# Kernel tuning notes

Measured on AMD Instinct MI355X. Metric: run time of the kernel, lower is better.

The kernel has to match this reference:

```python
import jax, jax.numpy as jnp
import numpy as np

V = 32000   # shared src/trg vocab size
E = 128     # EMB_DIM
H = 256     # HID_DIM
B = 32      # batch
S = 64      # src len
T = 64      # trg len


def setup_inputs() -> dict:
    key = jax.random.key(0)
    ks = jax.random.split(key, 16)
    s = 0.05
    n = lambda k, shape: jax.random.normal(k, shape, dtype=jnp.float32) * s
    return {
        "src": jax.random.randint(ks[0], (B, S), 0, V),
        "trg": jax.random.randint(ks[1], (B, T), 0, V),
        "enc_emb": n(ks[2], (V, E)),
        "enc_Wih": n(ks[3], (4 * H, E)),
        "enc_Whh": n(ks[4], (4 * H, H)),
        "enc_b": n(ks[5], (4 * H,)),   # b_ih + b_hh fused
        "dec_emb": n(ks[6], (V, E)),
        "dec_Wih": n(ks[7], (4 * H, E)),
        "dec_Whh": n(ks[8], (4 * H, H)),
        "dec_b": n(ks[9], (4 * H,)),
        "fc_W": n(ks[10], (V, H)),
        "fc_b": n(ks[11], (V,)),
    }


def _lstm_scan(x_seq, h0, c0, Wih, Whh, b):
    # x_seq: [T, B, E]; PyTorch gate order: i, f, g, o
    def step(carry, x):
        h, c = carry
        gates = x @ Wih.T + h @ Whh.T + b          # [B, 4H]
        i, f, g, o = jnp.split(gates, 4, axis=-1)
        c = jax.nn.sigmoid(f) * c + jax.nn.sigmoid(i) * jnp.tanh(g)
        h = jax.nn.sigmoid(o) * jnp.tanh(c)
        return (h, c), h
    (h, c), hs = jax.lax.scan(step, (h0, c0), x_seq)
    return h, c, hs


def reference(src, trg, enc_emb, enc_Wih, enc_Whh, enc_b,
              dec_emb, dec_Wih, dec_Whh, dec_b, fc_W, fc_b):
    dtype = enc_emb.dtype
    h0 = jnp.zeros((B, H), dtype)
    c0 = jnp.zeros((B, H), dtype)

    # Encoder: embed src, run LSTM, keep final (hidden, cell)
    src_e = enc_emb[src].transpose(1, 0, 2)        # [S, B, E]
    h, c, _ = _lstm_scan(src_e, h0, c0, enc_Wih, enc_Whh, enc_b)

    # Decoder with teacher_forcing_ratio=1.0: input at step t is trg[:, t-1]
    dec_in = dec_emb[trg[:, :-1]].transpose(1, 0, 2)   # [T-1, B, E]
    _, _, hs = _lstm_scan(dec_in, h, c, dec_Wih, dec_Whh, dec_b)  # [T-1, B, H]

    logits = hs @ fc_W.T + fc_b                    # [T-1, B, V]
    # outputs[:, 0, :] stays zero as in the torch code
    outputs = jnp.concatenate(
        [jnp.zeros((1, B, fc_W.shape[0]), dtype), logits], axis=0)
    return outputs.transpose(1, 0, 2)              # [B, T, V]
```

## Files before the change

kernel.cpp:

```cpp
#include <hip/hip_runtime.h>


typedef _Float16 f16x2 __attribute__((ext_vector_type(2)));
typedef short short8 __attribute__((ext_vector_type(8)));
typedef float f32x4 __attribute__((ext_vector_type(4)));
typedef unsigned long long u64;

#define DEV __device__ __forceinline__

static constexpr int Vv = 32000, Ee = 128, Hh = 256, Bb = 32, Ss = 64, Tt = 64;
static constexpr int G4 = 4 * Hh;
static constexpr int MR = (Tt - 1) * Bb;
static constexpr size_t OUT_BT = (size_t)Tt * Vv;

static constexpr size_t OFF_ENCPRE = 0;
static constexpr size_t OFF_DECPRE = OFF_ENCPRE + (size_t)Ss * Bb * G4 * 4;
static constexpr size_t OFF_WQE    = OFF_DECPRE + (size_t)(Tt - 1) * Bb * G4 * 4;
static constexpr size_t OFF_WQD    = OFF_WQE + (size_t)G4 * Hh * 2;
static constexpr size_t OFF_WPE    = OFF_WQD + (size_t)G4 * Hh * 2;
static constexpr size_t OFF_WPD    = OFF_WPE + (size_t)G4 * Ee * 4;
static constexpr size_t OFF_HW     = OFF_WPD + (size_t)G4 * Ee * 4;

DEV float sigm(float x) { return 1.0f / (1.0f + expf(-x)); }

DEV unsigned short f2bf(float x) {
  unsigned u = __float_as_uint(x);
  u = u + 0x7fffu + ((u >> 16) & 1u);
  return (unsigned short)(u >> 16);
}

DEV float dot2(unsigned wu, unsigned hu, float acc) {
  union { unsigned u; f16x2 v; } a, b;
  a.u = wu; b.u = hu;
#if __has_builtin(__builtin_amdgcn_fdot2)
  return __builtin_amdgcn_fdot2(a.v, b.v, acc, false);
#else
  return acc + (float)a.v.x * (float)b.v.x + (float)a.v.y * (float)b.v.y;
#endif
}

__global__ __launch_bounds__(256) void k_pack_whh(const float* __restrict__ src,
                                                  _Float16* __restrict__ dst) {
  int tid = blockIdx.x * 256 + threadIdx.x;
  if (tid >= G4 * Hh) return;
  int r = tid >> 8, k = tid & 255;
  dst[((size_t)(k >> 3) * G4 + r) * 8 + (k & 7)] = (_Float16)src[tid];
}

__global__ __launch_bounds__(256) void k_pack_wih(const float* __restrict__ src,
                                                  float* __restrict__ dst) {
  int tid = blockIdx.x * 256 + threadIdx.x;
  if (tid >= G4 * Ee) return;
  int g = tid >> 7, e = tid & 127;
  dst[((size_t)(e >> 2) * G4 + g) * 4 + (e & 3)] = src[tid];
}

__global__ __launch_bounds__(256) void k_init(u64* __restrict__ w) {
  w[blockIdx.x * 256 + threadIdx.x] = 0ull;
}

__global__ __launch_bounds__(1024) void k_pre(
    const int* __restrict__ src, const int* __restrict__ trg,
    const float* __restrict__ enc_emb, const float* __restrict__ dec_emb,
    const float* __restrict__ WpE, const float* __restrict__ WpD,
    const float* __restrict__ enc_b, const float* __restrict__ dec_b,
    float* __restrict__ enc_pre, float* __restrict__ dec_pre) {
  int blk = blockIdx.x;
  int step = blk >> 2;
  int b0 = (blk & 3) * 8;
  bool enc = step < Ss;
  int ts = enc ? step : step - Ss;
  const int*   tok  = enc ? src : trg;
  const float* emb  = enc ? enc_emb : dec_emb;
  const float* Wp   = enc ? WpE : WpD;
  const float* bias = enc ? enc_b : dec_b;
  float* pre = enc ? (enc_pre + ((size_t)step * Bb + b0) * G4)
                   : (dec_pre + ((size_t)(step - Ss) * Bb + b0) * G4);

  __shared__ __align__(16) float xs[8][128];
  int tid = threadIdx.x;
  {
    int bl = tid >> 7, e = tid & 127;
    int token = tok[(b0 + bl) * 64 + ts];
    xs[bl][e] = emb[(size_t)token * Ee + e];
  }
  __syncthreads();

  int g = tid;
  float acc[8];
  float bv = bias[g];
#pragma unroll
  for (int bb = 0; bb < 8; ++bb) acc[bb] = bv;

  const f32x4* w4 = (const f32x4*)Wp;
  const f32x4(*x4)[32] = (const f32x4(*)[32])xs;
#pragma unroll 4
  for (int e4 = 0; e4 < 32; ++e4) {
    f32x4 w = w4[(size_t)e4 * G4 + g];
#pragma unroll
    for (int bb = 0; bb < 8; ++bb) {
      f32x4 xv = x4[bb][e4];
      acc[bb] += w.x * xv.x + w.y * xv.y + w.z * xv.z + w.w * xv.w;
    }
  }
#pragma unroll
  for (int bb = 0; bb < 8; ++bb) pre[(size_t)bb * G4 + g] = acc[bb];
}

__global__ __launch_bounds__(256, 1) void k_lstm2(
    const float* __restrict__ enc_pre, const float* __restrict__ dec_pre,
    const _Float16* __restrict__ WqE, const _Float16* __restrict__ WqD,
    u64* __restrict__ hword, float* __restrict__ hs) {
  const int bid = blockIdx.x;
  const int j = bid >> 5, b = bid & 31;
  const int t = threadIdx.x;
  const int wv = t >> 6, l = t & 63;
  const int c_loc = l & 31, khalf = l >> 5;
  const int r_loc = wv * 32 + c_loc;
  const int row = wv * 256 + j * 32 + c_loc;

  __shared__ uint4 wlds[2][32][128];
  __shared__ unsigned hbits[128];
  __shared__ float gbuf[4][32];
  __shared__ float hstash[32];

  {
    const uint4* gE = (const uint4*)WqE + row;
    const uint4* gD = (const uint4*)WqD + row;
#pragma unroll 4
    for (int kk = 0; kk < 32; ++kk) wlds[0][kk][r_loc] = gE[(size_t)kk * G4];
#pragma unroll 4
    for (int kk = 0; kk < 32; ++kk) wlds[1][kk][r_loc] = gD[(size_t)kk * G4];
  }
  float c = 0.0f;
  __syncthreads();

  for (int step = 0; step < 127; ++step) {
    const bool enc = step < Ss;
    const float* pre = (enc ? enc_pre + (size_t)step * (Bb * G4)
                            : dec_pre + (size_t)(step - Ss) * (Bb * G4)) +
                       (size_t)b * G4;
    float pv = pre[row];

    if (t < 128) {
      if (step == 0) {
        hbits[t] = 0u;
      } else {
        u64* wp = hword + ((size_t)(step & 1) * 32 + b) * 128 + t;
        u64 v;
        do {
          v = __hip_atomic_load(wp, __ATOMIC_RELAXED, __HIP_MEMORY_SCOPE_AGENT);
        } while ((unsigned)(v >> 32) != (unsigned)step);
        hbits[t] = (unsigned)v;
      }
    }
    __syncthreads();

    const uint4* wl = &wlds[enc ? 0 : 1][khalf * 16][0];
    const uint4* hv4 = (const uint4*)hbits;
    float a0 = 0.f, a1 = 0.f, a2 = 0.f, a3 = 0.f;
#pragma unroll
    for (int k8 = 0; k8 < 16; ++k8) {
      uint4 w8 = wl[k8 * 128 + r_loc];
      uint4 h8 = hv4[khalf * 16 + k8];
      a0 = dot2(w8.x, h8.x, a0);
      a1 = dot2(w8.y, h8.y, a1);
      a2 = dot2(w8.z, h8.z, a2);
      a3 = dot2(w8.w, h8.w, a3);
    }
    float acc = (a0 + a1) + (a2 + a3);
    acc += __shfl_xor(acc, 32, 64);
    if (l < 32) gbuf[wv][c_loc] = acc + pv;
    __syncthreads();

    if (t < 32) {
      float gi = gbuf[0][t], gf = gbuf[1][t], gg = gbuf[2][t], go = gbuf[3][t];
      c = sigm(gf) * c + sigm(gi) * tanhf(gg);
      float hn = sigm(go) * tanhf(c);
      hstash[t] = hn;
      if (!enc) hs[((size_t)(step - Ss) * Bb + b) * Hh + j * 32 + t] = hn;
      if ((t & 1) == 0) {
        union { _Float16 f; unsigned short u; } u0, u1;
        u0.f = (_Float16)hn;
        u1.f = (_Float16)hstash[t + 1];
        u64 wd = ((u64)(unsigned)(step + 1) << 32) |
                 ((unsigned)u1.u << 16) | (unsigned)u0.u;
        __hip_atomic_store(
            hword + ((size_t)((step + 1) & 1) * 32 + b) * 128 + j * 16 + (t >> 1),
            wd, __ATOMIC_RELAXED, __HIP_MEMORY_SCOPE_AGENT);
      }
    }
  }
}

__global__ __launch_bounds__(256) void k_zero0(float* __restrict__ out) {
  int v = blockIdx.x * 256 + threadIdx.x;
  out[(size_t)blockIdx.y * OUT_BT + v] = 0.0f;
}

__global__ __launch_bounds__(256) void k_fc(const float* __restrict__ hs,
                                            const float* __restrict__ fcW,
                                            const float* __restrict__ fcb,
                                            float* __restrict__ out) {
  constexpr int LDH = 136;
  __shared__ __align__(16) unsigned short As[64 * LDH];
  __shared__ __align__(16) unsigned short Bs[64 * LDH];
  int n0 = blockIdx.x * 64, m0 = blockIdx.y * 64;
  int tid = threadIdx.x;
  int lane = tid & 63, wave = tid >> 6;
  int l15 = lane & 15, q = lane >> 4;
  int msub = (wave & 1) * 32, nsub = (wave >> 1) * 32;
  f32x4 acc[2][2] = {};

  for (int kb = 0; kb < 2; ++kb) {
#pragma unroll
    for (int r = 0; r < 4; ++r) {
      int vecid = tid + 256 * r;
      int i = vecid >> 4;
      int kk = (vecid & 15) * 8;
      int gk = kb * 128 + kk;
      short8 va, vb;
      int gm = m0 + i;
      if (gm < MR) {
        const float* p = hs + (size_t)gm * Hh + gk;
#pragma unroll
        for (int e = 0; e < 8; ++e) va[e] = (short)f2bf(p[e]);
      } else {
#pragma unroll
        for (int e = 0; e < 8; ++e) va[e] = 0;
      }
      const float* pb = fcW + (size_t)(n0 + i) * Hh + gk;
#pragma unroll
      for (int e = 0; e < 8; ++e) vb[e] = (short)f2bf(pb[e]);
      *(short8*)&As[i * LDH + kk] = va;
      *(short8*)&Bs[i * LDH + kk] = vb;
    }
    __syncthreads();
#pragma unroll
    for (int ks = 0; ks < 4; ++ks) {
      int koff = ks * 32 + q * 8;
      short8 a0 = *(const short8*)&As[(msub + l15) * LDH + koff];
      short8 a1 = *(const short8*)&As[(msub + 16 + l15) * LDH + koff];
      short8 b0 = *(const short8*)&Bs[(nsub + l15) * LDH + koff];
      short8 b1 = *(const short8*)&Bs[(nsub + 16 + l15) * LDH + koff];
      acc[0][0] = __builtin_amdgcn_mfma_f32_16x16x32_bf16(a0, b0, acc[0][0], 0, 0, 0);
      acc[0][1] = __builtin_amdgcn_mfma_f32_16x16x32_bf16(a0, b1, acc[0][1], 0, 0, 0);
      acc[1][0] = __builtin_amdgcn_mfma_f32_16x16x32_bf16(a1, b0, acc[1][0], 0, 0, 0);
      acc[1][1] = __builtin_amdgcn_mfma_f32_16x16x32_bf16(a1, b1, acc[1][1], 0, 0, 0);
    }
    __syncthreads();
  }
#pragma unroll
  for (int ni = 0; ni < 2; ++ni) {
    int gn = n0 + nsub + ni * 16 + l15;
    float bv = fcb[gn];
#pragma unroll
    for (int mi = 0; mi < 2; ++mi) {
#pragma unroll
      for (int r = 0; r < 4; ++r) {
        int gm = m0 + msub + mi * 16 + q * 4 + r;
        if (gm < MR) {
          int tt = gm >> 5, bb = gm & 31;
          out[(size_t)bb * OUT_BT + (size_t)(tt + 1) * Vv + gn] = acc[mi][ni][r] + bv;
        }
      }
    }
  }
}

extern "C" void kernel_launch(void* const* d_in, const int* in_sizes, int n_in,
                              void* d_out, int out_size, void* d_ws, size_t ws_size,
                              hipStream_t stream) {
  const int*   src     = (const int*)d_in[0];
  const int*   trg     = (const int*)d_in[1];
  const float* enc_emb = (const float*)d_in[2];
  const float* enc_Wih = (const float*)d_in[3];
  const float* enc_Whh = (const float*)d_in[4];
  const float* enc_b   = (const float*)d_in[5];
  const float* dec_emb = (const float*)d_in[6];
  const float* dec_Wih = (const float*)d_in[7];
  const float* dec_Whh = (const float*)d_in[8];
  const float* dec_b   = (const float*)d_in[9];
  const float* fc_W    = (const float*)d_in[10];
  const float* fc_b    = (const float*)d_in[11];
  float* out = (float*)d_out;

  char* ob = (char*)d_out;
  float*     enc_pre = (float*)(ob + OFF_ENCPRE);
  float*     dec_pre = (float*)(ob + OFF_DECPRE);
  _Float16*  WqE     = (_Float16*)(ob + OFF_WQE);
  _Float16*  WqD     = (_Float16*)(ob + OFF_WQD);
  float*     WpE     = (float*)(ob + OFF_WPE);
  float*     WpD     = (float*)(ob + OFF_WPD);
  u64*       hword   = (u64*)(ob + OFF_HW);
  float*     hs      = (float*)d_ws;

  k_init<<<32, 256, 0, stream>>>(hword);
  k_pack_whh<<<1024, 256, 0, stream>>>(enc_Whh, WqE);
  k_pack_whh<<<1024, 256, 0, stream>>>(dec_Whh, WqD);
  k_pack_wih<<<512, 256, 0, stream>>>(enc_Wih, WpE);
  k_pack_wih<<<512, 256, 0, stream>>>(dec_Wih, WpD);
  k_pre<<<508, 1024, 0, stream>>>(src, trg, enc_emb, dec_emb, WpE, WpD,
                                  enc_b, dec_b, enc_pre, dec_pre);
  k_lstm2<<<256, 256, 0, stream>>>(enc_pre, dec_pre, WqE, WqD, hword, hs);
  k_zero0<<<dim3(125, 32), 256, 0, stream>>>(out);
  k_fc<<<dim3(500, 32), 256, 0, stream>>>(hs, fc_W, fc_b, out);
}
```

Before: 750.4 us.

## Store decoder hiddens as bf16 and keep fc_W tile resident across M loop

The LSTM kernel now writes decoder hidden states directly as bf16, so the FC GEMM loads them without per-element fp32-to-bf16 conversion. The FC kernel shrinks from a 500x32 grid to 500 blocks. Each block converts its 64-row slice of fc_W to bf16 once into LDS with the full K=256 resident, then loops over all 32 M tiles. This removes the 32x redundant fp32 reads and conversions of fc_W, at the cost of far fewer blocks (500 vs 16000), a serial per-block M loop, and twice the LDS per block.

```diff
diff --git a/kernel.cpp b/kernel.cpp
--- a/kernel.cpp
+++ b/kernel.cpp
@@ -110,7 +110,7 @@
 __global__ __launch_bounds__(256, 1) void k_lstm2(
     const float* __restrict__ enc_pre, const float* __restrict__ dec_pre,
     const _Float16* __restrict__ WqE, const _Float16* __restrict__ WqD,
-    u64* __restrict__ hword, float* __restrict__ hs) {
+    u64* __restrict__ hword, unsigned short* __restrict__ hsb) {
   const int bid = blockIdx.x;
   const int j = bid >> 5, b = bid & 31;
   const int t = threadIdx.x;
@@ -178,7 +178,8 @@
       c = sigm(gf) * c + sigm(gi) * tanhf(gg);
       float hn = sigm(go) * tanhf(c);
       hstash[t] = hn;
-      if (!enc) hs[((size_t)(step - Ss) * Bb + b) * Hh + j * 32 + t] = hn;
+      if (!enc)
+        hsb[((size_t)(step - Ss) * Bb + b) * Hh + j * 32 + t] = f2bf(hn);
       if ((t & 1) == 0) {
         union { _Float16 f; unsigned short u; } u0, u1;
         u0.f = (_Float16)hn;
@@ -198,70 +199,74 @@
   out[(size_t)blockIdx.y * OUT_BT + v] = 0.0f;
 }
 
-__global__ __launch_bounds__(256) void k_fc(const float* __restrict__ hs,
+__global__ __launch_bounds__(256) void k_fc(const unsigned short* __restrict__ hsb,
                                             const float* __restrict__ fcW,
                                             const float* __restrict__ fcb,
                                             float* __restrict__ out) {
-  constexpr int LDH = 136;
-  __shared__ __align__(16) unsigned short As[64 * LDH];
-  __shared__ __align__(16) unsigned short Bs[64 * LDH];
-  int n0 = blockIdx.x * 64, m0 = blockIdx.y * 64;
+  constexpr int LDB = 264;
+  __shared__ __align__(16) unsigned short As[64 * LDB];
+  __shared__ __align__(16) unsigned short Bs[64 * LDB];
+  int n0 = blockIdx.x * 64;
   int tid = threadIdx.x;
   int lane = tid & 63, wave = tid >> 6;
   int l15 = lane & 15, q = lane >> 4;
   int msub = (wave & 1) * 32, nsub = (wave >> 1) * 32;
-  f32x4 acc[2][2] = {};
-
-  for (int kb = 0; kb < 2; ++kb) {
-#pragma unroll
-    for (int r = 0; r < 4; ++r) {
+
+#pragma unroll
+  for (int r = 0; r < 8; ++r) {
+    int vecid = tid + 256 * r;
+    int i = vecid >> 5;
+    int kk = (vecid & 31) * 8;
+    const float* pb = fcW + (size_t)(n0 + i) * Hh + kk;
+    short8 vb;
+#pragma unroll
+    for (int e = 0; e < 8; ++e) vb[e] = (short)f2bf(pb[e]);
+    *(short8*)&Bs[i * LDB + kk] = vb;
+  }
+  float bv0 = fcb[n0 + nsub + l15];
+  float bv1 = fcb[n0 + nsub + 16 + l15];
+
+  for (int mt = 0; mt < 32; ++mt) {
+    int m0 = mt * 64;
+    __syncthreads();
+#pragma unroll
+    for (int r = 0; r < 8; ++r) {
       int vecid = tid + 256 * r;
-      int i = vecid >> 4;
-      int kk = (vecid & 15) * 8;
-      int gk = kb * 128 + kk;
-      short8 va, vb;
+      int i = vecid >> 5;
+      int kk = (vecid & 31) * 8;
       int gm = m0 + i;
-      if (gm < MR) {
-        const float* p = hs + (size_t)gm * Hh + gk;
-#pragma unroll
-        for (int e = 0; e < 8; ++e) va[e] = (short)f2bf(p[e]);
-      } else {
-#pragma unroll
-        for (int e = 0; e < 8; ++e) va[e] = 0;
-      }
-      const float* pb = fcW + (size_t)(n0 + i) * Hh + gk;
-#pragma unroll
-      for (int e = 0; e < 8; ++e) vb[e] = (short)f2bf(pb[e]);
-      *(short8*)&As[i * LDH + kk] = va;
-      *(short8*)&Bs[i * LDH + kk] = vb;
+      short8 va = {};
+      if (gm < MR) va = *(const short8*)&hsb[(size_t)gm * Hh + kk];
+      *(short8*)&As[i * LDB + kk] = va;
     }
     __syncthreads();
-#pragma unroll
-    for (int ks = 0; ks < 4; ++ks) {
+
+    f32x4 acc[2][2] = {};
+#pragma unroll
+    for (int ks = 0; ks < 8; ++ks) {
       int koff = ks * 32 + q * 8;
-      short8 a0 = *(const short8*)&As[(msub + l15) * LDH + koff];
-      short8 a1 = *(const short8*)&As[(msub + 16 + l15) * LDH + koff];
-      short8 b0 = *(const short8*)&Bs[(nsub + l15) * LDH + koff];
-      short8 b1 = *(const short8*)&Bs[(nsub + 16 + l15) * LDH + koff];
+      short8 a0 = *(const short8*)&As[(msub + l15) * LDB + koff];
+      short8 a1 = *(const short8*)&As[(msub + 16 + l15) * LDB + koff];
+      short8 b0 = *(const short8*)&Bs[(nsub + l15) * LDB + koff];
+      short8 b1 = *(const short8*)&Bs[(nsub + 16 + l15) * LDB + koff];
       acc[0][0] = __builtin_amdgcn_mfma_f32_16x16x32_bf16(a0, b0, acc[0][0], 0, 0, 0);
       acc[0][1] = __builtin_amdgcn_mfma_f32_16x16x32_bf16(a0, b1, acc[0][1], 0, 0, 0);
       acc[1][0] = __builtin_amdgcn_mfma_f32_16x16x32_bf16(a1, b0, acc[1][0], 0, 0, 0);
       acc[1][1] = __builtin_amdgcn_mfma_f32_16x16x32_bf16(a1, b1, acc[1][1], 0, 0, 0);
     }
-    __syncthreads();
-  }
-#pragma unroll
-  for (int ni = 0; ni < 2; ++ni) {
-    int gn = n0 + nsub + ni * 16 + l15;
-    float bv = fcb[gn];
-#pragma unroll
-    for (int mi = 0; mi < 2; ++mi) {
-#pragma unroll
-      for (int r = 0; r < 4; ++r) {
-        int gm = m0 + msub + mi * 16 + q * 4 + r;
-        if (gm < MR) {
-          int tt = gm >> 5, bb = gm & 31;
-          out[(size_t)bb * OUT_BT + (size_t)(tt + 1) * Vv + gn] = acc[mi][ni][r] + bv;
+#pragma unroll
+    for (int ni = 0; ni < 2; ++ni) {
+      int gn = n0 + nsub + ni * 16 + l15;
+      float bv = ni ? bv1 : bv0;
+#pragma unroll
+      for (int mi = 0; mi < 2; ++mi) {
+#pragma unroll
+        for (int r = 0; r < 4; ++r) {
+          int gm = m0 + msub + mi * 16 + q * 4 + r;
+          if (gm < MR) {
+            int tt = gm >> 5, bb = gm & 31;
+            out[(size_t)bb * OUT_BT + (size_t)(tt + 1) * Vv + gn] = acc[mi][ni][r] + bv;
+          }
         }
       }
     }
@@ -293,7 +298,7 @@
   float*     WpE     = (float*)(ob + OFF_WPE);
   float*     WpD     = (float*)(ob + OFF_WPD);
   u64*       hword   = (u64*)(ob + OFF_HW);
-  float*     hs      = (float*)d_ws;
+  unsigned short* hsb = (unsigned short*)d_ws;
 
   k_init<<<32, 256, 0, stream>>>(hword);
   k_pack_whh<<<1024, 256, 0, stream>>>(enc_Whh, WqE);
@@ -302,7 +307,7 @@
   k_pack_wih<<<512, 256, 0, stream>>>(dec_Wih, WpD);
   k_pre<<<508, 1024, 0, stream>>>(src, trg, enc_emb, dec_emb, WpE, WpD,
                                   enc_b, dec_b, enc_pre, dec_pre);
-  k_lstm2<<<256, 256, 0, stream>>>(enc_pre, dec_pre, WqE, WqD, hword, hs);
+  k_lstm2<<<256, 256, 0, stream>>>(enc_pre, dec_pre, WqE, WqD, hword, hsb);
   k_zero0<<<dim3(125, 32), 256, 0, stream>>>(out);
-  k_fc<<<dim3(500, 32), 256, 0, stream>>>(hs, fc_W, fc_b, out);
-}
+  k_fc<<<dim3(500), 256, 0, stream>>>(hsb, fc_W, fc_b, out);
+}
```

Result: faster. 641.3 us (-14.5%).
